# Kernel tuning notes

Hardware: AMD Instinct MI355X
Metric: run time of the kernel (lower is better)

Reference implementation:

```python
import jax, jax.numpy as jnp
import numpy as np

E = 2048   # embedding_size
H = 2048   # hidden_size
B = 512    # batch
OUT = 2    # output_size (coords)


def setup_inputs() -> dict:
    key = jax.random.key(0)
    ks = jax.random.split(key, 11)
    s = 0.02
    return {
        "embedding": jax.random.normal(ks[0], (B, E), dtype=jnp.float32),
        "max_seq_length": 256,
        "W_embed": jax.random.normal(ks[1], (H, E), dtype=jnp.float32) * s,
        "b_embed": jnp.zeros((H,), dtype=jnp.float32),
        "W_ih": jax.random.normal(ks[2], (4 * H, OUT), dtype=jnp.float32) * s,
        "b_ih": jnp.zeros((4 * H,), dtype=jnp.float32),
        "W_hh": jax.random.normal(ks[3], (4 * H, H), dtype=jnp.float32) * s,
        "b_hh": jnp.zeros((4 * H,), dtype=jnp.float32),
        "W_out": jax.random.normal(ks[4], (OUT, H), dtype=jnp.float32) * s,
        "b_out": jnp.zeros((OUT,), dtype=jnp.float32),
        "W_stop": jax.random.normal(ks[5], (1, H), dtype=jnp.float32) * s,
        "b_stop": jnp.zeros((1,), dtype=jnp.float32),
    }


def reference(embedding, max_seq_length, W_embed, b_embed, W_ih, b_ih,
              W_hh, b_hh, W_out, b_out, W_stop, b_stop):
    # h_0 from embedding head (num_layers == 1)
    h0 = embedding @ W_embed.T + b_embed          # (B, H)
    c0 = jnp.zeros_like(h0)
    x0 = jnp.zeros((embedding.shape[0], OUT), dtype=embedding.dtype)

    def step(carry, _):
        h, c, x = carry
        gates = x @ W_ih.T + b_ih + h @ W_hh.T + b_hh    # (B, 4H)
        i, f, g, o = jnp.split(gates, 4, axis=-1)         # torch gate order i,f,g,o
        c = jax.nn.sigmoid(f) * c + jax.nn.sigmoid(i) * jnp.tanh(g)
        h = jax.nn.sigmoid(o) * jnp.tanh(c)
        coord = h @ W_out.T + b_out                        # (B, 2)
        stop = jax.nn.sigmoid(h @ W_stop.T + b_stop)       # (B, 1)
        return (h, c, coord), (coord, stop)

    _, (coords, stops) = jax.lax.scan(step, (h0, c0, x0), xs=None,
                                      length=max_seq_length)
    outputs = jnp.transpose(coords, (1, 0, 2))     # (B, T, 2)
    stop_probs = jnp.transpose(stops, (1, 0, 2))   # (B, T, 1)
    return outputs, stop_probs
```

## Files before the change

kernel.cpp:

```cpp
#include <hip/hip_runtime.h>
#include <stdint.h>

#define E_DIM 2048
#define H_DIM 2048
#define B_DIM 512
#define T_DIM 256
#define G4H   8192

typedef unsigned short u16;
typedef __attribute__((ext_vector_type(8))) short bf16x8;
typedef __attribute__((ext_vector_type(4))) float f32x4;

__device__ inline u16 f2b(float f) {
  union { float f; uint32_t i; } v; v.f = f;
  uint32_t u = v.i;
  return (u16)((u + 0x7FFFu + ((u >> 16) & 1u)) >> 16);
}
__device__ inline float b2f(u16 u) {
  union { uint32_t i; float f; } v; v.i = ((uint32_t)u) << 16; return v.f;
}

__device__ __forceinline__ void stage16(const void* g, void* l) {
  __builtin_amdgcn_global_load_lds(
      (const __attribute__((address_space(1))) uint32_t*)g,
      (__attribute__((address_space(3))) uint32_t*)l, 16, 0, 0);
}

__global__ __launch_bounds__(256) void convert_bf16(const float* __restrict__ s,
                                                    u16* __restrict__ d, int n4) {
  int i = blockIdx.x * 256 + threadIdx.x;
  if (i < n4) {
    float4 f = ((const float4*)s)[i];
    ushort4 o;
    o.x = f2b(f.x); o.y = f2b(f.y); o.z = f2b(f.z); o.w = f2b(f.w);
    ((ushort4*)d)[i] = o;
  }
}

__global__ __launch_bounds__(256) void build_weff(const float* __restrict__ W,
                                                  const float* __restrict__ W_ih,
                                                  const float* __restrict__ W_out,
                                                  u16* __restrict__ Wz) {
  int id = blockIdx.x * 256 + threadIdx.x;
  int lane = id & 63;
  int k32  = (id >> 6) & 63;
  int n16  = id >> 12;
  int np = n16 * 16 + (lane & 15);
  int k  = k32 * 32 + (lane >> 4) * 8;
  int g = np & 3, jrow = np >> 2;
  int src = g * H_DIM + jrow;
  float wi0 = W_ih[src * 2 + 0], wi1 = W_ih[src * 2 + 1];
  const float* sw = W + (size_t)src * H_DIM + k;
  u16 out[8];
  for (int j = 0; j < 8; ++j) {
    float v = sw[j] + wi0 * W_out[k + j] + wi1 * W_out[H_DIM + k + j];
    out[j] = f2b(v);
  }
  u16* dst = Wz + (size_t)id * 8;
  *(ushort4*)(dst) = *(ushort4*)&out[0];
  *(ushort4*)(dst + 4) = *(ushort4*)&out[4];
}

__global__ __launch_bounds__(256) void build_epi(const float* __restrict__ b_ih,
                                                 const float* __restrict__ b_hh,
                                                 const float* __restrict__ W_ih,
                                                 const float* __restrict__ b_out,
                                                 float* __restrict__ epi) {
  int np = blockIdx.x * 256 + threadIdx.x;
  int src = (np & 3) * H_DIM + (np >> 2);
  float wi0 = W_ih[src * 2 + 0], wi1 = W_ih[src * 2 + 1];
  float4 e;
  e.x = b_ih[src] + b_hh[src] + b_out[0] * wi0 + b_out[1] * wi1;
  e.y = wi0;
  e.z = wi1;
  e.w = 0.f;
  ((float4*)epi)[np] = e;
}

#define BM 64
#define BN 128
#define BK 32
__global__ __launch_bounds__(256) void gemm_bt(const u16* __restrict__ A,
                                               const u16* __restrict__ Bm,
                                               float* __restrict__ C,
                                               int M, int N, int K) {
  __shared__ u16 sA[BM * BK];
  __shared__ u16 sB[BN * BK];
  const int t = threadIdx.x;
  const int bm0 = blockIdx.y * BM, bn0 = blockIdx.x * BN;
  const int wave = t >> 6, lane = t & 63;
  const int wm = (wave >> 1) * 32, wn = (wave & 1) * 64;
  const int r16 = lane & 15, quad = lane >> 4;

  f32x4 acc[2][4];
  const f32x4 z = {0.f, 0.f, 0.f, 0.f};
  for (int i = 0; i < 2; ++i)
    for (int j = 0; j < 4; ++j) acc[i][j] = z;

  const int arow = t >> 2, acg = t & 3;

  for (int k0 = 0; k0 < K; k0 += BK) {
    __syncthreads();
    *(uint4*)&sA[arow * BK + acg * 8] =
        *(const uint4*)&A[(size_t)(bm0 + arow) * K + k0 + acg * 8];
    for (int i = 0; i < 2; ++i) {
      int c = t + 256 * i;
      int row = c >> 2, cg = c & 3;
      *(uint4*)&sB[row * BK + cg * 8] =
          *(const uint4*)&Bm[(size_t)(bn0 + row) * K + k0 + cg * 8];
    }
    __syncthreads();
    bf16x8 af[2], bfr[4];
    for (int mt = 0; mt < 2; ++mt)
      af[mt] = *(const bf16x8*)&sA[(wm + mt * 16 + r16) * BK + quad * 8];
    for (int nt = 0; nt < 4; ++nt)
      bfr[nt] = *(const bf16x8*)&sB[(wn + nt * 16 + r16) * BK + quad * 8];
    for (int mt = 0; mt < 2; ++mt)
      for (int nt = 0; nt < 4; ++nt)
        acc[mt][nt] = __builtin_amdgcn_mfma_f32_16x16x32_bf16(af[mt], bfr[nt],
                                                              acc[mt][nt], 0, 0, 0);
  }
  for (int mt = 0; mt < 2; ++mt)
    for (int nt = 0; nt < 4; ++nt) {
      int row = bm0 + wm + mt * 16 + quad * 4;
      int col = bn0 + wn + nt * 16 + r16;
      for (int r = 0; r < 4; ++r)
        C[(size_t)(row + r) * N + col] = acc[mt][nt][r];
    }
}

__global__ __launch_bounds__(256) void init_state(const float* __restrict__ h0pre,
                                                  const float* __restrict__ b_embed,
                                                  u16* __restrict__ h,
                                                  float* __restrict__ c,
                                                  float* __restrict__ xzero) {
  int idx = blockIdx.x * 256 + threadIdx.x;
  int bg = idx >> 11, k = idx & (H_DIM - 1);
  float v = h0pre[idx] + b_embed[k];
  size_t chunk = (((size_t)(bg >> 4)) * 64 + (k >> 5)) * 64 + ((k >> 3) & 3) * 16 + (bg & 15);
  size_t pos = chunk * 8 + (k & 7);
  h[pos] = f2b(v);
  c[pos] = 0.f;
  if (idx < B_DIM * 2) xzero[idx] = 0.f;
}

__global__ __launch_bounds__(64) void calc_xcorr(const float* __restrict__ h0pre,
                                                 const float* __restrict__ b_embed,
                                                 const float* __restrict__ W_out,
                                                 const float* __restrict__ b_out,
                                                 float* __restrict__ xc) {
  int m = blockIdx.x, ln = threadIdx.x;
  float s0 = 0.f, s1 = 0.f;
  for (int k = ln; k < H_DIM; k += 64) {
    float hv = h0pre[(size_t)m * H_DIM + k] + b_embed[k];
    s0 += hv * W_out[k];
    s1 += hv * W_out[H_DIM + k];
  }
  for (int off = 32; off > 0; off >>= 1) {
    s0 += __shfl_down(s0, off);
    s1 += __shfl_down(s1, off);
  }
  if (ln == 0) {
    xc[m * 2 + 0] = -(s0 + b_out[0]);
    xc[m * 2 + 1] = -(s1 + b_out[1]);
  }
}

__global__ __launch_bounds__(256) void init_out(const float* __restrict__ b_out,
                                                const float* __restrict__ b_stop,
                                                float* __restrict__ coords,
                                                float* __restrict__ stops) {
  int i = blockIdx.x * 256 + threadIdx.x;
  coords[i * 2 + 0] = b_out[0];
  coords[i * 2 + 1] = b_out[1];
  stops[i] = b_stop[0];
}

__global__ __launch_bounds__(256) void finalize_stops(float* __restrict__ stops) {
  int i = blockIdx.x * 256 + threadIdx.x;
  stops[i] = 1.f / (1.f + __expf(-stops[i]));
}

__global__ __launch_bounds__(512, 2) void gemm_lstm(const u16* __restrict__ hA,
                                                 const u16* __restrict__ Wz,
                                                 const float* __restrict__ epi,
                                                 const float* __restrict__ x,
                                                 float* __restrict__ c,
                                                 u16* __restrict__ h_out,
                                                 const float* __restrict__ W_out,
                                                 const float* __restrict__ W_stop,
                                                 float* __restrict__ coords,
                                                 float* __restrict__ stops,
                                                 int trow) {
  __shared__ __align__(16) char smem[131072];

  const int bid = blockIdx.x;
  const int nt = (bid & 7) * 8 + ((bid >> 3) & 7);
  const int mt = bid >> 6;
  const int bm0 = mt * 128;

  const int t = threadIdx.x, wv = t >> 6, ln = t & 63;
  const int kq = wv >> 2, wm = (wv >> 1) & 1, wn = wv & 1;
  const int r16 = ln & 15, quad = ln >> 4;

  const u16* gptr[4];
  uint32_t ldsoff[4];
#pragma unroll
  for (int s = 0; s < 4; ++s) {
    int ti = wv * 4 + s;
    int kqg = (ti >> 4) & 1, isB = (ti >> 3) & 1, rowi = ti & 7;
    int kc0 = kqg * 32;
    if (isB)
      gptr[s] = Wz + ((size_t)(nt * 8 + rowi) * 64 + kc0) * 512 + ln * 8;
    else
      gptr[s] = hA + ((size_t)((bm0 >> 4) + rowi) * 64 + kc0) * 512 + ln * 8;
    ldsoff[s] = (uint32_t)(kqg * 16384 + isB * 8192 + rowi * 1024);
  }

  f32x4 acc[4][4];
  const f32x4 z = {0.f, 0.f, 0.f, 0.f};
#pragma unroll
  for (int i = 0; i < 4; ++i)
#pragma unroll
    for (int j = 0; j < 4; ++j) acc[i][j] = z;

  const uint32_t rdbase = (uint32_t)(kq * 16384);

#define STAGE_PH(pp)                                                          \
  do {                                                                        \
    const uint32_t _bb = ((uint32_t)(pp) & 3u) * 32768u;                      \
    const size_t _go = (size_t)(pp) * 512;                                    \
    _Pragma("unroll")                                                         \
    for (int s = 0; s < 4; ++s)                                               \
      stage16(gptr[s] + _go, smem + (_bb + ldsoff[s]));                       \
  } while (0)

#define COMPUTE_PH(pp)                                                        \
  do {                                                                        \
    const char* _rb = smem + ((uint32_t)(pp) & 3u) * 32768u + rdbase;         \
    bf16x8 _af[4], _bf[4];                                                    \
    _Pragma("unroll")                                                         \
    for (int i = 0; i < 4; ++i)                                               \
      _af[i] = *(const bf16x8*)(_rb + (wm * 4 + i) * 1024 + ln * 16);         \
    _Pragma("unroll")                                                         \
    for (int i = 0; i < 4; ++i)                                               \
      _bf[i] = *(const bf16x8*)(_rb + 8192 + (wn * 4 + i) * 1024 + ln * 16);  \
    _Pragma("unroll")                                                         \
    for (int mi = 0; mi < 4; ++mi)                                            \
      _Pragma("unroll")                                                       \
      for (int ni = 0; ni < 4; ++ni)                                          \
        acc[mi][ni] = __builtin_amdgcn_mfma_f32_16x16x32_bf16(                \
            _af[mi], _bf[ni], acc[mi][ni], 0, 0, 0);                          \
  } while (0)

  STAGE_PH(0);
  STAGE_PH(1);
  STAGE_PH(2);

#pragma unroll 4
  for (int p = 0; p < 29; ++p) {
    asm volatile("s_waitcnt vmcnt(8)" ::: "memory");
    __builtin_amdgcn_s_barrier();
    STAGE_PH(p + 3);
    COMPUTE_PH(p);
  }
  asm volatile("s_waitcnt vmcnt(8)" ::: "memory");
  __builtin_amdgcn_s_barrier();
  COMPUTE_PH(29);
  asm volatile("s_waitcnt vmcnt(4)" ::: "memory");
  __builtin_amdgcn_s_barrier();
  COMPUTE_PH(30);
  asm volatile("s_waitcnt vmcnt(0)" ::: "memory");
  __builtin_amdgcn_s_barrier();
  COMPUTE_PH(31);
  __syncthreads();

#undef STAGE_PH
#undef COMPUTE_PH

  float* cb = (float*)smem;
  if (kq == 1) {
    float* dst = cb + (wm * 2 + wn) * 4096;
#pragma unroll
    for (int mi = 0; mi < 4; ++mi)
#pragma unroll
      for (int ni = 0; ni < 4; ++ni)
        *(f32x4*)&dst[((mi * 4 + ni) * 64 + ln) * 4] = acc[mi][ni];
  }
  __syncthreads();
  if (kq == 0) {
    const float* src = cb + (wm * 2 + wn) * 4096;
#pragma unroll
    for (int mi = 0; mi < 4; ++mi)
#pragma unroll
      for (int ni = 0; ni < 4; ++ni)
        acc[mi][ni] += *(const f32x4*)&src[((mi * 4 + ni) * 64 + ln) * 4];
  }
  __syncthreads();

  float* gt = (float*)smem;
  if (kq == 0) {
#pragma unroll
    for (int mi = 0; mi < 4; ++mi)
#pragma unroll
      for (int ni = 0; ni < 4; ++ni) {
        int row = wm * 64 + mi * 16 + quad * 4;
        int col = wn * 64 + ni * 16 + r16;
        f32x4 v = acc[mi][ni];
#pragma unroll
        for (int r = 0; r < 4; ++r)
          gt[(row + r) * 132 + col] = v[r];
      }
  }
  __syncthreads();

  {
    const int lrow = wv * 16 + r16;
    const int bg = bm0 + lrow;
    const float x0 = x[bg * 2 + 0], x1 = x[bg * 2 + 1];
    const size_t chunk = (((size_t)(bg >> 4)) * 64 + nt) * 64 + ln;
    const int hc0 = nt * 32 + quad * 8;
    float cv[8]; u16 hv[8];
    float s0 = 0.f, s1 = 0.f, s2 = 0.f;
    const float4* epi4 = (const float4*)epi;
    f32x4 cold0 = *(const f32x4*)&c[chunk * 8 + 0];
    f32x4 cold1 = *(const f32x4*)&c[chunk * 8 + 4];
#pragma unroll
    for (int j = 0; j < 8; ++j) {
      int col = quad * 32 + j * 4;
      float4 g4 = *(const float4*)&gt[lrow * 132 + col];
      float4 e0 = epi4[nt * 128 + col + 0];
      float4 e1 = epi4[nt * 128 + col + 1];
      float4 e2 = epi4[nt * 128 + col + 2];
      float4 e3 = epi4[nt * 128 + col + 3];
      float gi = g4.x + e0.x + x0 * e0.y + x1 * e0.z;
      float gf = g4.y + e1.x + x0 * e1.y + x1 * e1.z;
      float gg = g4.z + e2.x + x0 * e2.y + x1 * e2.z;
      float go = g4.w + e3.x + x0 * e3.y + x1 * e3.z;
      float si = 1.f / (1.f + __expf(-gi));
      float sf = 1.f / (1.f + __expf(-gf));
      float so = 1.f / (1.f + __expf(-go));
      float cold = (j < 4) ? cold0[j & 3] : cold1[j & 3];
      float cn = sf * cold + si * tanhf(gg);
      cv[j] = cn;
      float hf = so * tanhf(cn);
      hv[j] = f2b(hf);
      s0 += hf * W_out[hc0 + j];
      s1 += hf * W_out[H_DIM + hc0 + j];
      s2 += hf * W_stop[hc0 + j];
    }
    *(float4*)&c[chunk * 8 + 0] = *(float4*)&cv[0];
    *(float4*)&c[chunk * 8 + 4] = *(float4*)&cv[4];
    *(ushort4*)&h_out[chunk * 8 + 0] = *(ushort4*)&hv[0];
    *(ushort4*)&h_out[chunk * 8 + 4] = *(ushort4*)&hv[4];
    s0 += __shfl_xor(s0, 16); s1 += __shfl_xor(s1, 16); s2 += __shfl_xor(s2, 16);
    s0 += __shfl_xor(s0, 32); s1 += __shfl_xor(s1, 32); s2 += __shfl_xor(s2, 32);
    if (quad == 0) {
      atomicAdd(&coords[((size_t)bg * T_DIM + trow) * 2 + 0], s0);
      atomicAdd(&coords[((size_t)bg * T_DIM + trow) * 2 + 1], s1);
      atomicAdd(&stops[(size_t)bg * T_DIM + trow], s2);
    }
  }
}

extern "C" void kernel_launch(void* const* d_in, const int* in_sizes, int n_in,
                              void* d_out, int out_size, void* d_ws, size_t ws_size,
                              hipStream_t stream) {
  const float* embedding = (const float*)d_in[0];
  const float* W_embed   = (const float*)d_in[2];
  const float* b_embed   = (const float*)d_in[3];
  const float* W_ih      = (const float*)d_in[4];
  const float* b_ih      = (const float*)d_in[5];
  const float* W_hh      = (const float*)d_in[6];
  const float* b_hh      = (const float*)d_in[7];
  const float* W_out     = (const float*)d_in[8];
  const float* b_out     = (const float*)d_in[9];
  const float* W_stop    = (const float*)d_in[10];
  const float* b_stop    = (const float*)d_in[11];

  float* coords = (float*)d_out;
  float* stops  = (float*)d_out + (size_t)B_DIM * T_DIM * 2;

  char* ws = (char*)d_ws;
  u16* W_z     = (u16*)ws;   ws += (size_t)G4H * H_DIM * 2;
  u16* W_emb_b = (u16*)ws;   ws += (size_t)H_DIM * E_DIM * 2;
  u16* emb_b   = (u16*)ws;   ws += (size_t)B_DIM * E_DIM * 2;
  float* h0pre = (float*)ws; ws += (size_t)B_DIM * H_DIM * 4;
  float* epi   = (float*)ws; ws += (size_t)G4H * 4 * 4;
  float* cbuf  = (float*)ws; ws += (size_t)B_DIM * H_DIM * 4;
  u16* hbuf0   = (u16*)ws;   ws += (size_t)B_DIM * H_DIM * 2;
  u16* hbuf1   = (u16*)ws;   ws += (size_t)B_DIM * H_DIM * 2;
  float* xcorr = (float*)ws; ws += (size_t)B_DIM * 2 * 4;
  float* xzero = (float*)ws; ws += (size_t)B_DIM * 2 * 4;

  convert_bf16<<<(B_DIM * E_DIM / 4 + 255) / 256, 256, 0, stream>>>(embedding, emb_b, B_DIM * E_DIM / 4);
  convert_bf16<<<(H_DIM * E_DIM / 4 + 255) / 256, 256, 0, stream>>>(W_embed, W_emb_b, H_DIM * E_DIM / 4);
  build_weff<<<(G4H * H_DIM / 8) / 256, 256, 0, stream>>>(W_hh, W_ih, W_out, W_z);
  build_epi<<<G4H / 256, 256, 0, stream>>>(b_ih, b_hh, W_ih, b_out, epi);
  init_out<<<(B_DIM * T_DIM) / 256, 256, 0, stream>>>(b_out, b_stop, coords, stops);

  gemm_bt<<<dim3(H_DIM / BN, B_DIM / BM), 256, 0, stream>>>(emb_b, W_emb_b, h0pre,
                                                            B_DIM, H_DIM, E_DIM);
  init_state<<<(B_DIM * H_DIM) / 256, 256, 0, stream>>>(h0pre, b_embed, hbuf0, cbuf, xzero);
  calc_xcorr<<<B_DIM, 64, 0, stream>>>(h0pre, b_embed, W_out, b_out, xcorr);

  for (int t = 0; t < T_DIM; ++t) {
    u16* h_in  = (t & 1) ? hbuf1 : hbuf0;
    u16* h_out = (t & 1) ? hbuf0 : hbuf1;
    const float* xv = (t == 0) ? xcorr : xzero;
    gemm_lstm<<<256, 512, 0, stream>>>(h_in, W_z, epi, xv, cbuf, h_out,
                                       W_out, W_stop, coords, stops, t);
  }
  finalize_stops<<<(B_DIM * T_DIM) / 256, 256, 0, stream>>>(stops);
}
```

Measured before the change: 7.014 ms.

## Retile recurrent LSTM GEMM to 64x128 blocks with 256 threads and triple buffering

```diff
diff --git a/kernel.cpp b/kernel.cpp
--- a/kernel.cpp
+++ b/kernel.cpp
@@ -181,7 +181,7 @@
   stops[i] = 1.f / (1.f + __expf(-stops[i]));
 }
 
-__global__ __launch_bounds__(512, 2) void gemm_lstm(const u16* __restrict__ hA,
+__global__ __launch_bounds__(256, 2) void gemm_lstm(const u16* __restrict__ hA,
                                                  const u16* __restrict__ Wz,
                                                  const float* __restrict__ epi,
                                                  const float* __restrict__ x,
@@ -192,29 +192,32 @@
                                                  float* __restrict__ coords,
                                                  float* __restrict__ stops,
                                                  int trow) {
-  __shared__ __align__(16) char smem[131072];
+  __shared__ __align__(16) char smem[73728];
 
   const int bid = blockIdx.x;
   const int nt = (bid & 7) * 8 + ((bid >> 3) & 7);
   const int mt = bid >> 6;
-  const int bm0 = mt * 128;
+  const int bm0 = mt * 64;
 
   const int t = threadIdx.x, wv = t >> 6, ln = t & 63;
-  const int kq = wv >> 2, wm = (wv >> 1) & 1, wn = wv & 1;
+  const int kq = wv >> 1, wn = wv & 1;
   const int r16 = ln & 15, quad = ln >> 4;
 
-  const u16* gptr[4];
-  uint32_t ldsoff[4];
-#pragma unroll
-  for (int s = 0; s < 4; ++s) {
-    int ti = wv * 4 + s;
-    int kqg = (ti >> 4) & 1, isB = (ti >> 3) & 1, rowi = ti & 7;
-    int kc0 = kqg * 32;
-    if (isB)
-      gptr[s] = Wz + ((size_t)(nt * 8 + rowi) * 64 + kc0) * 512 + ln * 8;
-    else
-      gptr[s] = hA + ((size_t)((bm0 >> 4) + rowi) * 64 + kc0) * 512 + ln * 8;
-    ldsoff[s] = (uint32_t)(kqg * 16384 + isB * 8192 + rowi * 1024);
+  const u16* gptr[6];
+  uint32_t ldsoff[6];
+#pragma unroll
+  for (int s = 0; s < 6; ++s) {
+    int ti = wv * 6 + s;
+    if (ti < 8) {
+      int kqg = ti >> 2, rowi = ti & 3;
+      gptr[s] = hA + ((size_t)(mt * 4 + rowi) * 64 + kqg * 32) * 512 + ln * 8;
+      ldsoff[s] = (uint32_t)(kqg * 4096 + rowi * 1024);
+    } else {
+      int tb = ti - 8;
+      int kqg = tb >> 3, rowi = tb & 7;
+      gptr[s] = Wz + ((size_t)(nt * 8 + rowi) * 64 + kqg * 32) * 512 + ln * 8;
+      ldsoff[s] = (uint32_t)(8192 + kqg * 8192 + rowi * 1024);
+    }
   }
 
   f32x4 acc[4][4];
@@ -224,63 +227,63 @@
 #pragma unroll
     for (int j = 0; j < 4; ++j) acc[i][j] = z;
 
-  const uint32_t rdbase = (uint32_t)(kq * 16384);
-
-#define STAGE_PH(pp)                                                          \
+  const uint32_t rdA = (uint32_t)(kq * 4096);
+  const uint32_t rdB = (uint32_t)(8192 + kq * 8192 + wn * 4096);
+  const uint32_t ln16 = (uint32_t)(ln * 16);
+
+#define STAGE_PH(pp, bb)                                                      \
   do {                                                                        \
-    const uint32_t _bb = ((uint32_t)(pp) & 3u) * 32768u;                      \
     const size_t _go = (size_t)(pp) * 512;                                    \
     _Pragma("unroll")                                                         \
-    for (int s = 0; s < 4; ++s)                                               \
-      stage16(gptr[s] + _go, smem + (_bb + ldsoff[s]));                       \
+    for (int s = 0; s < 6; ++s)                                               \
+      stage16(gptr[s] + _go, smem + ((uint32_t)(bb) + ldsoff[s]));            \
   } while (0)
 
-#define COMPUTE_PH(pp)                                                        \
+#define COMP_PH(bb)                                                           \
   do {                                                                        \
-    const char* _rb = smem + ((uint32_t)(pp) & 3u) * 32768u + rdbase;         \
+    const char* _rb = smem + (uint32_t)(bb);                                  \
     bf16x8 _af[4], _bf[4];                                                    \
     _Pragma("unroll")                                                         \
     for (int i = 0; i < 4; ++i)                                               \
-      _af[i] = *(const bf16x8*)(_rb + (wm * 4 + i) * 1024 + ln * 16);         \
+      _af[i] = *(const bf16x8*)(_rb + rdA + i * 1024 + ln16);                 \
     _Pragma("unroll")                                                         \
     for (int i = 0; i < 4; ++i)                                               \
-      _bf[i] = *(const bf16x8*)(_rb + 8192 + (wn * 4 + i) * 1024 + ln * 16);  \
+      _bf[i] = *(const bf16x8*)(_rb + rdB + i * 1024 + ln16);                 \
+    __builtin_amdgcn_s_setprio(1);                                            \
     _Pragma("unroll")                                                         \
     for (int mi = 0; mi < 4; ++mi)                                            \
       _Pragma("unroll")                                                       \
       for (int ni = 0; ni < 4; ++ni)                                          \
         acc[mi][ni] = __builtin_amdgcn_mfma_f32_16x16x32_bf16(                \
             _af[mi], _bf[ni], acc[mi][ni], 0, 0, 0);                          \
+    __builtin_amdgcn_s_setprio(0);                                            \
   } while (0)
 
-  STAGE_PH(0);
-  STAGE_PH(1);
-  STAGE_PH(2);
-
-#pragma unroll 4
-  for (int p = 0; p < 29; ++p) {
-    asm volatile("s_waitcnt vmcnt(8)" ::: "memory");
-    __builtin_amdgcn_s_barrier();
-    STAGE_PH(p + 3);
-    COMPUTE_PH(p);
-  }
-  asm volatile("s_waitcnt vmcnt(8)" ::: "memory");
-  __builtin_amdgcn_s_barrier();
-  COMPUTE_PH(29);
-  asm volatile("s_waitcnt vmcnt(4)" ::: "memory");
-  __builtin_amdgcn_s_barrier();
-  COMPUTE_PH(30);
-  asm volatile("s_waitcnt vmcnt(0)" ::: "memory");
-  __builtin_amdgcn_s_barrier();
-  COMPUTE_PH(31);
+#define VW6 asm volatile("s_waitcnt vmcnt(6)" ::: "memory")
+#define VW0 asm volatile("s_waitcnt vmcnt(0)" ::: "memory")
+#define BAR __builtin_amdgcn_s_barrier()
+
+  STAGE_PH(0, 0);
+  STAGE_PH(1, 24576);
+
+  for (int p = 0; p < 30; p += 3) {
+    VW6; BAR; STAGE_PH(p + 2, 49152); COMP_PH(0);
+    VW6; BAR; STAGE_PH(p + 3, 0);     COMP_PH(24576);
+    VW6; BAR; STAGE_PH(p + 4, 24576); COMP_PH(49152);
+  }
+  VW6; BAR; COMP_PH(0);
+  VW0; BAR; COMP_PH(24576);
   __syncthreads();
 
 #undef STAGE_PH
-#undef COMPUTE_PH
+#undef COMP_PH
+#undef VW6
+#undef VW0
+#undef BAR
 
   float* cb = (float*)smem;
   if (kq == 1) {
-    float* dst = cb + (wm * 2 + wn) * 4096;
+    float* dst = cb + wn * 4096;
 #pragma unroll
     for (int mi = 0; mi < 4; ++mi)
 #pragma unroll
@@ -289,7 +292,7 @@
   }
   __syncthreads();
   if (kq == 0) {
-    const float* src = cb + (wm * 2 + wn) * 4096;
+    const float* src = cb + wn * 4096;
 #pragma unroll
     for (int mi = 0; mi < 4; ++mi)
 #pragma unroll
@@ -304,7 +307,7 @@
     for (int mi = 0; mi < 4; ++mi)
 #pragma unroll
       for (int ni = 0; ni < 4; ++ni) {
-        int row = wm * 64 + mi * 16 + quad * 4;
+        int row = mi * 16 + quad * 4;
         int col = wn * 64 + ni * 16 + r16;
         f32x4 v = acc[mi][ni];
 #pragma unroll
@@ -408,7 +411,7 @@
     u16* h_in  = (t & 1) ? hbuf1 : hbuf0;
     u16* h_out = (t & 1) ? hbuf0 : hbuf1;
     const float* xv = (t == 0) ? xcorr : xzero;
-    gemm_lstm<<<256, 512, 0, stream>>>(h_in, W_z, epi, xv, cbuf, h_out,
+    gemm_lstm<<<512, 256, 0, stream>>>(h_in, W_z, epi, xv, cbuf, h_out,
                                        W_out, W_stop, coords, stops, t);
   }
   finalize_stops<<<(B_DIM * T_DIM) / 256, 256, 0, stream>>>(stops);
```

After: 7.403 ms. 5.5% more time.
